# Kernel optimization log

Measured on AMD Instinct MI355X. Metric: run time of the kernel, lower is better.

Reference implementation:

```python
import jax, jax.numpy as jnp
import numpy as np

A, H, HI = 4, 3, 2  # nagents, n_pol_heads, n_intr_rew_heads (sep_extr_head=True)
# leave-one-out index table: row i lists all agents k != i, in ascending order (torch loop order)
LOO = np.array([[k for k in range(A) if k != i] for i in range(A)])  # [A, A-1]


def setup_inputs() -> dict:
    key = jax.random.key(0)
    ks = jax.random.split(key, 12)
    B, S, C, D = 32768, 256, 16, 128  # batch, vect_state_size, action_size, hidden_dim
    IN = C * (A - 1) + D  # 176 critic input dim
    r = lambda k, shp, s=0.05: jax.random.normal(k, shp, dtype=jnp.float32) * s
    return {
        "state_vect": jax.random.normal(ks[0], (B, S), dtype=jnp.float32),
        "acs": jax.random.normal(ks[1], (A, H, B, C), dtype=jnp.float32),
        "enc_W": r(ks[2], (S, D)),
        "enc_b": r(ks[3], (D,)),
        "extr_W1": r(ks[4], (H, A, IN, D)),
        "extr_b1": r(ks[5], (H, A, D)),
        "extr_W2": r(ks[6], (H, A, D, C)),
        "extr_b2": r(ks[7], (H, A, C)),
        "intr_W1": r(ks[8], (HI, A, IN, D)),
        "intr_b1": r(ks[9], (HI, A, D)),
        "intr_W2": r(ks[10], (HI, A, D, C)),
        "intr_b2": r(ks[11], (HI, A, C)),
    }


def reference(state_vect, acs, enc_W, enc_b, extr_W1, extr_b1, extr_W2, extr_b2,
              intr_W1, intr_b1, intr_W2, intr_b2):
    B, C = acs.shape[2], acs.shape[3]
    D = enc_W.shape[1]
    # shared state encoder: Linear -> ReLU
    enc = jax.nn.relu(state_vect @ enc_W + enc_b)  # [B, D]
    # leave-one-out action concat per (agent, head): cat(acs[k!=i, j]) ++ enc
    rel = acs[LOO]                                 # [A, A-1, H, B, C]
    rel = rel.transpose(0, 2, 3, 1, 4).reshape(A, H, B, (A - 1) * C)
    x = jnp.concatenate([rel, jnp.broadcast_to(enc, (A, H, B, D))], axis=-1)  # [A,H,B,IN]
    # greedy action index of agent i's own head-j policy output
    int_acs = jnp.argmax(acs, axis=-1)             # [A, H, B]

    def critic(xin, W1, b1, W2, b2):
        # xin: [A, Hc, B, IN]; W1: [Hc, A, IN, D]; W2: [Hc, A, D, C]
        h = jax.nn.relu(jnp.einsum('ahbi,haid->ahbd', xin, W1)
                        + b1.transpose(1, 0, 2)[:, :, None, :])
        return (jnp.einsum('ahbd,hadc->ahbc', h, W2)
                + b2.transpose(1, 0, 2)[:, :, None, :])  # [A, Hc, B, C]

    extr_all_q = critic(x, extr_W1, extr_b1, extr_W2, extr_b2)          # [A,H,B,C]
    extr_q = jnp.take_along_axis(extr_all_q, int_acs[..., None], axis=-1)  # [A,H,B,1]
    # intr critics exist only for heads j>=1 (sep_extr_head=True -> offset -1)
    intr_all_q = critic(x[:, 1:], intr_W1, intr_b1, intr_W2, intr_b2)   # [A,HI,B,C]
    intr_q = jnp.take_along_axis(intr_all_q, int_acs[:, 1:, :, None], axis=-1)  # [A,HI,B,1]
    return extr_q, intr_q
```

## Files before the change

### kernel.cpp

```cpp
#include <hip/hip_runtime.h>

#define NA 4
#define NH 3
#define NHI 2
#define Bsz 32768
#define Ssz 256
#define Csz 16
#define Dsz 128
#define INsz 176
#define NP 20
#define KP 192

typedef __bf16 v8bf __attribute__((ext_vector_type(8)));
typedef float v4f __attribute__((ext_vector_type(4)));

#define OFF_ENC    0
#define OFF_ACSBF  8388608
#define OFF_W1F    20971520
#define OFF_ENCWF  21954560
#define OFF_W2T    22020096
#define OFF_AMX    22102016
#define OFF_ZERO   22495232

#define N_ACSROW (NA*NH*Bsz)
#define N_W1F   (NP*192*32)
#define N_ENCWF (256*32)
#define N_W2T   (NP*Csz*Dsz)
#define N_ZERO  16
#define N_PREP  (N_ACSROW+N_W1F+N_ENCWF+N_W2T+N_ZERO)

__global__ __launch_bounds__(256) void prep_kernel(
    const float* __restrict__ acs, const float* __restrict__ encW,
    const float* __restrict__ eW1, const float* __restrict__ iW1,
    const float* __restrict__ eW2, const float* __restrict__ iW2,
    char* __restrict__ ws)
{
    long tid = (long)blockIdx.x * 256 + threadIdx.x;

    if (tid < N_ACSROW) {
        const float4* src = (const float4*)(acs + (size_t)tid * 16);
        float4 f0 = src[0], f1 = src[1], f2 = src[2], f3 = src[3];
        float v[16] = {f0.x,f0.y,f0.z,f0.w, f1.x,f1.y,f1.z,f1.w,
                       f2.x,f2.y,f2.z,f2.w, f3.x,f3.y,f3.z,f3.w};
        v8bf o0, o1;
        #pragma unroll
        for (int i = 0; i < 8; ++i) { o0[i] = (__bf16)v[i]; o1[i] = (__bf16)v[8 + i]; }
        v8bf* dst = (v8bf*)(ws + OFF_ACSBF) + tid * 2;
        dst[0] = o0; dst[1] = o1;
        float best = v[0]; int bi = 0;
        #pragma unroll
        for (int c = 1; c < 16; ++c) if (v[c] > best) { best = v[c]; bi = c; }
        ((unsigned char*)(ws + OFF_AMX))[tid] = (unsigned char)bi;
        return;
    }
    tid -= N_ACSROW;
    if (tid < N_W1F) {
        const int n4 = (int)(tid & 31) * 4;
        const int k  = (int)((tid >> 5) % 192);
        const int p  = (int)(tid / 6144);
        const float* W1;
        if (p < 12) { int ai = p / 3, hj = p % 3; W1 = eW1 + (size_t)(hj * NA + ai) * INsz * Dsz; }
        else { int qq = p - 12; int ai = qq >> 1, jj = qq & 1; W1 = iW1 + (size_t)(jj * NA + ai) * INsz * Dsz; }
        float4 f = (k < INsz) ? *(const float4*)(W1 + (size_t)k * Dsz + n4)
                              : (float4){0.f, 0.f, 0.f, 0.f};
        const int kc = k >> 5, q = (k >> 3) & 3, j = k & 7;
        __bf16* dst = (__bf16*)(ws + OFF_W1F);
        const float fv[4] = {f.x, f.y, f.z, f.w};
        #pragma unroll
        for (int i = 0; i < 4; ++i) {
            const int n = n4 + i, nt = n >> 4, m = n & 15;
            dst[((size_t)(p * 6 + kc) * 8 + nt) * 512 + (q * 16 + m) * 8 + j] = (__bf16)fv[i];
        }
        return;
    }
    tid -= N_W1F;
    if (tid < N_ENCWF) {
        const int n4 = (int)(tid & 31) * 4;
        const int k  = (int)(tid >> 5);
        float4 f = *(const float4*)(encW + (size_t)k * Dsz + n4);
        const int kc = k >> 5, q = (k >> 3) & 3, j = k & 7;
        __bf16* dst = (__bf16*)(ws + OFF_ENCWF);
        const float fv[4] = {f.x, f.y, f.z, f.w};
        #pragma unroll
        for (int i = 0; i < 4; ++i) {
            const int n = n4 + i, nt = n >> 4, m = n & 15;
            dst[((size_t)kc * 8 + nt) * 512 + (q * 16 + m) * 8 + j] = (__bf16)fv[i];
        }
        return;
    }
    tid -= N_ENCWF;
    if (tid < N_W2T) {
        int d = (int)(tid & 127);
        int rest = (int)(tid >> 7);
        int c = rest & 15, p = rest >> 4;
        const float* W2;
        if (p < 12) { int ai = p / 3, hj = p % 3; W2 = eW2 + (size_t)(hj * NA + ai) * Dsz * Csz; }
        else { int qq = p - 12; int ai = qq >> 1, jj = qq & 1; W2 = iW2 + (size_t)(jj * NA + ai) * Dsz * Csz; }
        ((__bf16*)(ws + OFF_W2T))[(size_t)p * Csz * Dsz + (size_t)c * Dsz + d] = (__bf16)W2[(size_t)d * Csz + c];
        return;
    }
    tid -= N_W2T;
    if (tid < N_ZERO) ((float*)(ws + OFF_ZERO))[tid] = 0.f;
}

__global__ __launch_bounds__(256) void enc_kernel(const float* __restrict__ sv,
                                                  const float* __restrict__ encb,
                                                  char* __restrict__ ws)
{
    const int t = threadIdx.x;
    const int wv = t >> 6, lane = t & 63, m = lane & 15, q = lane >> 4;
    const int R = blockIdx.x * 64 + wv * 16 + m;
    const __bf16* encwf = (const __bf16*)(ws + OFF_ENCWF);
    __bf16* enc = (__bf16*)(ws + OFF_ENC);

    v4f acc[8];
    #pragma unroll
    for (int nt = 0; nt < 8; ++nt) acc[nt] = (v4f){0.f, 0.f, 0.f, 0.f};

    const float* arow = sv + (size_t)R * Ssz + q * 8;
    #pragma unroll
    for (int kc = 0; kc < 8; ++kc) {
        float4 f0 = *(const float4*)(arow + kc * 32);
        float4 f1 = *(const float4*)(arow + kc * 32 + 4);
        v8bf af;
        af[0]=(__bf16)f0.x; af[1]=(__bf16)f0.y; af[2]=(__bf16)f0.z; af[3]=(__bf16)f0.w;
        af[4]=(__bf16)f1.x; af[5]=(__bf16)f1.y; af[6]=(__bf16)f1.z; af[7]=(__bf16)f1.w;
        #pragma unroll
        for (int nt = 0; nt < 8; ++nt) {
            v8bf bf = *(const v8bf*)(encwf + ((size_t)kc * 8 + nt) * 512 + lane * 8);
            acc[nt] = __builtin_amdgcn_mfma_f32_16x16x32_bf16(af, bf, acc[nt], 0, 0, 0);
        }
    }
    const int rbase = blockIdx.x * 64 + wv * 16 + q * 4;
    #pragma unroll
    for (int nt = 0; nt < 8; ++nt) {
        const float bias = encb[nt * 16 + m];
        #pragma unroll
        for (int rg = 0; rg < 4; ++rg) {
            float v = acc[nt][rg] + bias;
            v = v > 0.f ? v : 0.f;
            enc[(size_t)(rbase + rg) * Dsz + nt * 16 + m] = (__bf16)v;
        }
    }
}

__global__ __launch_bounds__(256, 3) void critic_kernel(
    const float* __restrict__ eb1, const float* __restrict__ eb2,
    const float* __restrict__ ib1, const float* __restrict__ ib2,
    const char* __restrict__ ws, float* __restrict__ out)
{
    __shared__ __bf16 w1s[6 * 8 * 512];

    const int t = threadIdx.x;
    const int p  = blockIdx.y;
    const int rb = blockIdx.x;
    const int wv = t >> 6, lane = t & 63, m = lane & 15, q = lane >> 4;
    const int rw = rb * 128 + wv * 32;

    int ai, hj;
    const float *b1, *b2;
    float* outp;
    if (p < 12) {
        ai = p / 3; hj = p % 3;
        const int wi = hj * NA + ai;
        b1 = eb1 + (size_t)wi * Dsz; b2 = eb2 + (size_t)wi * Csz;
        outp = out + (size_t)(ai * NH + hj) * Bsz;
    } else {
        const int qq = p - 12; ai = qq >> 1; const int jj = qq & 1; hj = jj + 1;
        const int wi = jj * NA + ai;
        b1 = ib1 + (size_t)wi * Dsz; b2 = ib2 + (size_t)wi * Csz;
        outp = out + (size_t)NA * NH * Bsz + (size_t)(ai * NHI + jj) * Bsz;
    }

    const __bf16* acsb = (const __bf16*)(ws + OFF_ACSBF);
    const __bf16* encp = (const __bf16*)(ws + OFF_ENC);
    const __bf16* w1f  = (const __bf16*)(ws + OFF_W1F) + (size_t)p * 6 * 8 * 512;
    const __bf16* w2t  = (const __bf16*)(ws + OFF_W2T) + (size_t)p * Csz * Dsz;
    const unsigned char* amx = (const unsigned char*)(ws + OFF_AMX) + (size_t)(ai * NH + hj) * Bsz + rw;
    const __bf16* zerop = (const __bf16*)(ws + OFF_ZERO);

    {
        const v8bf* src = (const v8bf*)w1f;
        v8bf* dst = (v8bf*)w1s;
        #pragma unroll
        for (int i = 0; i < 12; ++i)
            dst[i * 256 + t] = src[i * 256 + t];
    }

    const int loo0 = 0 + (0 >= ai), loo1 = 1 + (1 >= ai), loo2 = 2 + (2 >= ai);
    const __bf16* a0p = acsb + (size_t)(loo0 * NH + hj) * Bsz * Csz;
    const __bf16* a1p = acsb + (size_t)(loo1 * NH + hj) * Bsz * Csz;
    const __bf16* a2p = acsb + (size_t)(loo2 * NH + hj) * Bsz * Csz;

    const int R0 = rw + m;
    const __bf16* base[6];
    int strd[6];
    base[0] = (q < 2) ? (a0p + (size_t)R0 * Csz + q * 8) : (a1p + (size_t)R0 * Csz + (q - 2) * 8);
    strd[0] = Csz;
    base[1] = (q < 2) ? (a2p + (size_t)R0 * Csz + q * 8) : (encp + (size_t)R0 * Dsz + (q - 2) * 8);
    strd[1] = (q < 2) ? Csz : Dsz;
    base[2] = encp + (size_t)R0 * Dsz + 16 + q * 8;  strd[2] = Dsz;
    base[3] = encp + (size_t)R0 * Dsz + 48 + q * 8;  strd[3] = Dsz;
    base[4] = encp + (size_t)R0 * Dsz + 80 + q * 8;  strd[4] = Dsz;
    base[5] = (q < 2) ? (encp + (size_t)R0 * Dsz + 112 + q * 8) : zerop;
    strd[5] = (q < 2) ? Dsz : 0;

    v4f acc[2][8];
    #pragma unroll
    for (int i = 0; i < 2; ++i)
        #pragma unroll
        for (int j = 0; j < 8; ++j)
            acc[i][j] = (v4f){0.f, 0.f, 0.f, 0.f};

    __syncthreads();

    #pragma unroll
    for (int kc = 0; kc < 6; ++kc) {
        v8bf af[2];
        #pragma unroll
        for (int mt = 0; mt < 2; ++mt)
            af[mt] = *(const v8bf*)(base[kc] + (size_t)(mt * 16) * strd[kc]);
        #pragma unroll
        for (int nt = 0; nt < 8; ++nt) {
            v8bf bf = *(const v8bf*)&w1s[((size_t)kc * 8 + nt) * 512 + lane * 8];
            acc[0][nt] = __builtin_amdgcn_mfma_f32_16x16x32_bf16(af[0], bf, acc[0][nt], 0, 0, 0);
            acc[1][nt] = __builtin_amdgcn_mfma_f32_16x16x32_bf16(af[1], bf, acc[1][nt], 0, 0, 0);
        }
    }

    float b1v[8];
    #pragma unroll
    for (int nt = 0; nt < 8; ++nt) b1v[nt] = b1[nt * 16 + m];

    #pragma unroll
    for (int mt = 0; mt < 2; ++mt) {
        const int rowb = mt * 16 + q * 4;
        const unsigned int cw = *(const unsigned int*)(amx + rowb);
        #pragma unroll
        for (int rg = 0; rg < 4; ++rg) {
            const int c = (cw >> (8 * rg)) & 255;
            const __bf16* wc = w2t + (size_t)c * Dsz + m;
            float partial = 0.f;
            #pragma unroll
            for (int nt = 0; nt < 8; ++nt) {
                float h = acc[mt][nt][rg] + b1v[nt];
                h = h > 0.f ? h : 0.f;
                partial += h * (float)wc[nt * 16];
            }
            partial += __shfl_xor(partial, 1, 64);
            partial += __shfl_xor(partial, 2, 64);
            partial += __shfl_xor(partial, 4, 64);
            partial += __shfl_xor(partial, 8, 64);
            if (m == 0)
                outp[rw + rowb + rg] = partial + b2[c];
        }
    }
}

extern "C" void kernel_launch(void* const* d_in, const int* in_sizes, int n_in,
                              void* d_out, int out_size, void* d_ws, size_t ws_size,
                              hipStream_t stream) {
    const float* sv   = (const float*)d_in[0];
    const float* acs  = (const float*)d_in[1];
    const float* encW = (const float*)d_in[2];
    const float* encb = (const float*)d_in[3];
    const float* eW1  = (const float*)d_in[4];
    const float* eb1  = (const float*)d_in[5];
    const float* eW2  = (const float*)d_in[6];
    const float* eb2  = (const float*)d_in[7];
    const float* iW1  = (const float*)d_in[8];
    const float* ib1  = (const float*)d_in[9];
    const float* iW2  = (const float*)d_in[10];
    const float* ib2  = (const float*)d_in[11];
    float* out = (float*)d_out;
    char* ws = (char*)d_ws;

    hipLaunchKernelGGL(prep_kernel, dim3((N_PREP + 255) / 256), dim3(256), 0, stream,
                       acs, encW, eW1, iW1, eW2, iW2, ws);
    hipLaunchKernelGGL(enc_kernel, dim3(Bsz / 64), dim3(256), 0, stream, sv, encb, ws);
    hipLaunchKernelGGL(critic_kernel, dim3(Bsz / 128, NP), dim3(256), 0, stream,
                       eb1, eb2, ib1, ib2, ws, out);
}
```

Measured before the change: 176.9 us.

## Retile critic kernel to 512 rows per block with pipelined A-fragment loads

Each critic block now handles 512 rows: each wave covers four 16-row tiles over two iterations, and the next K-chunk's A fragments are loaded while the current chunk's MFMAs run. The encoder output is stored in an MFMA-fragment-tiled layout through an LDS transpose, and W2 is repacked and staged in padded LDS for the argmax-gather epilogue. The aim is to load W1 into LDS fewer times per row, issue wider contiguous global loads and hide load latency. The cost is more accumulator registers (launch bounds lowered to 2 blocks per SM) and a quarter as many blocks.

```diff
diff --git a/kernel.cpp b/kernel.cpp
--- a/kernel.cpp
+++ b/kernel.cpp
@@ -10,6 +10,7 @@
 #define INsz 176
 #define NP 20
 #define KP 192
+#define GT 2
 
 typedef __bf16 v8bf __attribute__((ext_vector_type(8)));
 typedef float v4f __attribute__((ext_vector_type(4)));
@@ -96,7 +97,8 @@
         const float* W2;
         if (p < 12) { int ai = p / 3, hj = p % 3; W2 = eW2 + (size_t)(hj * NA + ai) * Dsz * Csz; }
         else { int qq = p - 12; int ai = qq >> 1, jj = qq & 1; W2 = iW2 + (size_t)(jj * NA + ai) * Dsz * Csz; }
-        ((__bf16*)(ws + OFF_W2T))[(size_t)p * Csz * Dsz + (size_t)c * Dsz + d] = (__bf16)W2[(size_t)d * Csz + c];
+        ((__bf16*)(ws + OFF_W2T))[(size_t)p * 2048 + c * 128 + (d & 15) * 8 + (d >> 4)]
+            = (__bf16)W2[(size_t)d * Csz + c];
         return;
     }
     tid -= N_W2T;
@@ -107,11 +109,13 @@
                                                   const float* __restrict__ encb,
                                                   char* __restrict__ ws)
 {
+    __shared__ __bf16 tb[4][16 * 136];
+
     const int t = threadIdx.x;
     const int wv = t >> 6, lane = t & 63, m = lane & 15, q = lane >> 4;
     const int R = blockIdx.x * 64 + wv * 16 + m;
     const __bf16* encwf = (const __bf16*)(ws + OFF_ENCWF);
-    __bf16* enc = (__bf16*)(ws + OFF_ENC);
+    char* enct = ws + OFF_ENC;
 
     v4f acc[8];
     #pragma unroll
@@ -131,7 +135,6 @@
             acc[nt] = __builtin_amdgcn_mfma_f32_16x16x32_bf16(af, bf, acc[nt], 0, 0, 0);
         }
     }
-    const int rbase = blockIdx.x * 64 + wv * 16 + q * 4;
     #pragma unroll
     for (int nt = 0; nt < 8; ++nt) {
         const float bias = encb[nt * 16 + m];
@@ -139,23 +142,45 @@
         for (int rg = 0; rg < 4; ++rg) {
             float v = acc[nt][rg] + bias;
             v = v > 0.f ? v : 0.f;
-            enc[(size_t)(rbase + rg) * Dsz + nt * 16 + m] = (__bf16)v;
-        }
+            tb[wv][(q * 4 + rg) * 136 + nt * 16 + m] = (__bf16)v;
+        }
+    }
+    __syncthreads();
+    const int rt = blockIdx.x * 4 + wv;
+    #pragma unroll
+    for (int kc = 0; kc < 4; ++kc) {
+        v8bf v = *(const v8bf*)&tb[wv][m * 136 + kc * 32 + q * 8];
+        *(v8bf*)(enct + ((size_t)(rt * 4 + kc) * 64 + lane) * 16) = v;
     }
 }
 
-__global__ __launch_bounds__(256, 3) void critic_kernel(
+#define LD_AF(D, KC, GG) \
+  { _Pragma("unroll") \
+    for (int mt_ = 0; mt_ < 4; ++mt_) \
+      D[mt_] = *(const v8bf*)(base[KC] + (size_t)((mt_ + 16 * (GG)) * strd[KC])); }
+
+#define MFMA_KC(AF, KC) \
+  { _Pragma("unroll") \
+    for (int nt_ = 0; nt_ < 8; ++nt_) { \
+      v8bf bf_ = *(const v8bf*)&w1s[(size_t)(((KC) * 8 + nt_) * 512) + lane * 8]; \
+      acc[0][nt_] = __builtin_amdgcn_mfma_f32_16x16x32_bf16(AF[0], bf_, acc[0][nt_], 0, 0, 0); \
+      acc[1][nt_] = __builtin_amdgcn_mfma_f32_16x16x32_bf16(AF[1], bf_, acc[1][nt_], 0, 0, 0); \
+      acc[2][nt_] = __builtin_amdgcn_mfma_f32_16x16x32_bf16(AF[2], bf_, acc[2][nt_], 0, 0, 0); \
+      acc[3][nt_] = __builtin_amdgcn_mfma_f32_16x16x32_bf16(AF[3], bf_, acc[3][nt_], 0, 0, 0); \
+    } }
+
+__global__ __launch_bounds__(256, 2) void critic_kernel(
     const float* __restrict__ eb1, const float* __restrict__ eb2,
     const float* __restrict__ ib1, const float* __restrict__ ib2,
     const char* __restrict__ ws, float* __restrict__ out)
 {
     __shared__ __bf16 w1s[6 * 8 * 512];
+    __shared__ __bf16 w2s[16 * 136];
 
     const int t = threadIdx.x;
     const int p  = blockIdx.y;
     const int rb = blockIdx.x;
     const int wv = t >> 6, lane = t & 63, m = lane & 15, q = lane >> 4;
-    const int rw = rb * 128 + wv * 32;
 
     int ai, hj;
     const float *b1, *b2;
@@ -172,87 +197,97 @@
         outp = out + (size_t)NA * NH * Bsz + (size_t)(ai * NHI + jj) * Bsz;
     }
 
-    const __bf16* acsb = (const __bf16*)(ws + OFF_ACSBF);
-    const __bf16* encp = (const __bf16*)(ws + OFF_ENC);
-    const __bf16* w1f  = (const __bf16*)(ws + OFF_W1F) + (size_t)p * 6 * 8 * 512;
-    const __bf16* w2t  = (const __bf16*)(ws + OFF_W2T) + (size_t)p * Csz * Dsz;
-    const unsigned char* amx = (const unsigned char*)(ws + OFF_AMX) + (size_t)(ai * NH + hj) * Bsz + rw;
-    const __bf16* zerop = (const __bf16*)(ws + OFF_ZERO);
+    const char* acsb = ws + OFF_ACSBF;
+    const char* enct = ws + OFF_ENC;
+    const __bf16* w1f = (const __bf16*)(ws + OFF_W1F) + (size_t)p * 6 * 8 * 512;
+    const __bf16* w2t = (const __bf16*)(ws + OFF_W2T) + (size_t)p * 2048;
+    const unsigned char* amxp = (const unsigned char*)(ws + OFF_AMX)
+        + (size_t)(ai * NH + hj) * Bsz + (size_t)rb * 512 + wv * 64;
+    const char* zerop = ws + OFF_ZERO;
 
     {
         const v8bf* src = (const v8bf*)w1f;
-        v8bf* dst = (v8bf*)w1s;
         #pragma unroll
         for (int i = 0; i < 12; ++i)
-            dst[i * 256 + t] = src[i * 256 + t];
+            ((v8bf*)w1s)[i * 256 + t] = src[i * 256 + t];
+        v8bf wv2 = ((const v8bf*)w2t)[t];
+        *(v8bf*)&w2s[(t >> 4) * 136 + (t & 15) * 8] = wv2;
     }
 
     const int loo0 = 0 + (0 >= ai), loo1 = 1 + (1 >= ai), loo2 = 2 + (2 >= ai);
-    const __bf16* a0p = acsb + (size_t)(loo0 * NH + hj) * Bsz * Csz;
-    const __bf16* a1p = acsb + (size_t)(loo1 * NH + hj) * Bsz * Csz;
-    const __bf16* a2p = acsb + (size_t)(loo2 * NH + hj) * Bsz * Csz;
-
-    const int R0 = rw + m;
-    const __bf16* base[6];
+    const size_t rowoff = ((size_t)rb * 512 + wv * 64 + m) * 32;
+    const char* pl0 = acsb + (size_t)(loo0 * NH + hj) * Bsz * 32 + rowoff;
+    const char* pl1 = acsb + (size_t)(loo1 * NH + hj) * Bsz * 32 + rowoff;
+    const char* pl2 = acsb + (size_t)(loo2 * NH + hj) * Bsz * 32 + rowoff;
+    const int rt0 = rb * 32 + wv * 4;
+    const char* encB = enct + (size_t)rt0 * 4096 + m * 16;
+
+    const char* base[6];
     int strd[6];
-    base[0] = (q < 2) ? (a0p + (size_t)R0 * Csz + q * 8) : (a1p + (size_t)R0 * Csz + (q - 2) * 8);
-    strd[0] = Csz;
-    base[1] = (q < 2) ? (a2p + (size_t)R0 * Csz + q * 8) : (encp + (size_t)R0 * Dsz + (q - 2) * 8);
-    strd[1] = (q < 2) ? Csz : Dsz;
-    base[2] = encp + (size_t)R0 * Dsz + 16 + q * 8;  strd[2] = Dsz;
-    base[3] = encp + (size_t)R0 * Dsz + 48 + q * 8;  strd[3] = Dsz;
-    base[4] = encp + (size_t)R0 * Dsz + 80 + q * 8;  strd[4] = Dsz;
-    base[5] = (q < 2) ? (encp + (size_t)R0 * Dsz + 112 + q * 8) : zerop;
-    strd[5] = (q < 2) ? Dsz : 0;
-
-    v4f acc[2][8];
-    #pragma unroll
-    for (int i = 0; i < 2; ++i)
+    base[0] = (q < 2) ? (pl0 + q * 16) : (pl1 + (q - 2) * 16);           strd[0] = 512;
+    base[1] = (q < 2) ? (pl2 + q * 16) : (encB + (q - 2) * 256);         strd[1] = (q < 2) ? 512 : 4096;
+    base[2] = encB + (q + 2)  * 256;                                     strd[2] = 4096;
+    base[3] = encB + (q + 6)  * 256;                                     strd[3] = 4096;
+    base[4] = encB + (q + 10) * 256;                                     strd[4] = 4096;
+    base[5] = (q < 2) ? (encB + (14 + q) * 256) : zerop;                 strd[5] = (q < 2) ? 4096 : 0;
+
+    float b1v[8];
+    #pragma unroll
+    for (int nt = 0; nt < 8; ++nt) b1v[nt] = b1[nt * 16 + m];
+
+    v4f acc[4][8];
+    #pragma unroll
+    for (int i = 0; i < 4; ++i)
         #pragma unroll
         for (int j = 0; j < 8; ++j)
             acc[i][j] = (v4f){0.f, 0.f, 0.f, 0.f};
 
+    v8bf afA[4], afB[4];
+    LD_AF(afA, 0, 0)
+
     __syncthreads();
 
     #pragma unroll
-    for (int kc = 0; kc < 6; ++kc) {
-        v8bf af[2];
-        #pragma unroll
-        for (int mt = 0; mt < 2; ++mt)
-            af[mt] = *(const v8bf*)(base[kc] + (size_t)(mt * 16) * strd[kc]);
-        #pragma unroll
-        for (int nt = 0; nt < 8; ++nt) {
-            v8bf bf = *(const v8bf*)&w1s[((size_t)kc * 8 + nt) * 512 + lane * 8];
-            acc[0][nt] = __builtin_amdgcn_mfma_f32_16x16x32_bf16(af[0], bf, acc[0][nt], 0, 0, 0);
-            acc[1][nt] = __builtin_amdgcn_mfma_f32_16x16x32_bf16(af[1], bf, acc[1][nt], 0, 0, 0);
-        }
-    }
-
-    float b1v[8];
-    #pragma unroll
-    for (int nt = 0; nt < 8; ++nt) b1v[nt] = b1[nt * 16 + m];
-
-    #pragma unroll
-    for (int mt = 0; mt < 2; ++mt) {
-        const int rowb = mt * 16 + q * 4;
-        const unsigned int cw = *(const unsigned int*)(amx + rowb);
-        #pragma unroll
-        for (int rg = 0; rg < 4; ++rg) {
-            const int c = (cw >> (8 * rg)) & 255;
-            const __bf16* wc = w2t + (size_t)c * Dsz + m;
-            float partial = 0.f;
+    for (int g = 0; g < GT; ++g) {
+        unsigned int cw[4];
+        #pragma unroll
+        for (int mt = 0; mt < 4; ++mt)
+            cw[mt] = *(const unsigned int*)(amxp + g * 256 + mt * 16 + q * 4);
+
+        LD_AF(afB, 1, g)  MFMA_KC(afA, 0)
+        LD_AF(afA, 2, g)  MFMA_KC(afB, 1)
+        LD_AF(afB, 3, g)  MFMA_KC(afA, 2)
+        LD_AF(afA, 4, g)  MFMA_KC(afB, 3)
+        LD_AF(afB, 5, g)  MFMA_KC(afA, 4)
+        if (g + 1 < GT) { LD_AF(afA, 0, g + 1) }
+        MFMA_KC(afB, 5)
+
+        #pragma unroll
+        for (int mt = 0; mt < 4; ++mt) {
+            const unsigned int cwv = cw[mt];
             #pragma unroll
-            for (int nt = 0; nt < 8; ++nt) {
-                float h = acc[mt][nt][rg] + b1v[nt];
-                h = h > 0.f ? h : 0.f;
-                partial += h * (float)wc[nt * 16];
+            for (int rg = 0; rg < 4; ++rg) {
+                const int c = (cwv >> (8 * rg)) & 255;
+                const v8bf w2v = *(const v8bf*)&w2s[c * 136 + m * 8];
+                float partial = 0.f;
+                #pragma unroll
+                for (int nt = 0; nt < 8; ++nt) {
+                    float h = acc[mt][nt][rg] + b1v[nt];
+                    h = h > 0.f ? h : 0.f;
+                    partial += h * (float)w2v[nt];
+                }
+                partial += __shfl_xor(partial, 1, 64);
+                partial += __shfl_xor(partial, 2, 64);
+                partial += __shfl_xor(partial, 4, 64);
+                partial += __shfl_xor(partial, 8, 64);
+                if (m == 0)
+                    outp[(size_t)rb * 512 + g * 256 + wv * 64 + mt * 16 + q * 4 + rg]
+                        = partial + b2[c];
             }
-            partial += __shfl_xor(partial, 1, 64);
-            partial += __shfl_xor(partial, 2, 64);
-            partial += __shfl_xor(partial, 4, 64);
-            partial += __shfl_xor(partial, 8, 64);
-            if (m == 0)
-                outp[rw + rowb + rg] = partial + b2[c];
+            if (g + 1 < GT) {
+                #pragma unroll
+                for (int nt = 0; nt < 8; ++nt) acc[mt][nt] = (v4f){0.f, 0.f, 0.f, 0.f};
+            }
         }
     }
 }
@@ -278,6 +313,6 @@
     hipLaunchKernelGGL(prep_kernel, dim3((N_PREP + 255) / 256), dim3(256), 0, stream,
                        acs, encW, eW1, iW1, eW2, iW2, ws);
     hipLaunchKernelGGL(enc_kernel, dim3(Bsz / 64), dim3(256), 0, stream, sv, encb, ws);
-    hipLaunchKernelGGL(critic_kernel, dim3(Bsz / 128, NP), dim3(256), 0, stream,
+    hipLaunchKernelGGL(critic_kernel, dim3(Bsz / 512, NP), dim3(256), 0, stream,
                        eb1, eb2, ib1, ib2, ws, out);
 }
```

New measurement: 170.5 us. 1.04x faster.
